# Kernel tuning notes

Measured on AMD Instinct MI355X. Metric: run time of the kernel, lower is better.

## Reference

```python
import jax, jax.numpy as jnp
import numpy as np

D_MODEL = 512
N_HEADS = 8
D_K = D_MODEL // N_HEADS


def setup_inputs() -> dict:
    key = jax.random.key(0)
    ks = jax.random.split(key, 12)
    B, L = 2, 512
    s = 1.0 / np.sqrt(D_MODEL)
    sk = 1.0 / np.sqrt(D_K)
    return {
        "query": jax.random.normal(ks[0], (B, L, D_MODEL), jnp.float32),
        "key": jax.random.normal(ks[1], (B, L, D_MODEL), jnp.float32),
        "value": jax.random.normal(ks[2], (B, L, D_MODEL), jnp.float32),
        "Wq": jax.random.normal(ks[3], (D_MODEL, D_MODEL), jnp.float32) * s,
        "bq": jnp.zeros((D_MODEL,), jnp.float32),
        "Wk": jax.random.normal(ks[4], (D_MODEL, D_MODEL), jnp.float32) * s,
        "bk": jnp.zeros((D_MODEL,), jnp.float32),
        "Wv": jax.random.normal(ks[5], (D_MODEL, D_MODEL), jnp.float32) * s,
        "bv": jnp.zeros((D_MODEL,), jnp.float32),
        "Wo": jax.random.normal(ks[6], (D_MODEL, D_MODEL), jnp.float32) * s,
        "bo": jnp.zeros((D_MODEL,), jnp.float32),
        "Aq": jax.random.normal(ks[7], (D_K, D_K), jnp.float32) * sk,  # inner W_q (no bias)
        "Ak": jax.random.normal(ks[8], (D_K, D_K), jnp.float32) * sk,  # inner W_k (no bias)
        "av": jax.random.normal(ks[9], (D_K,), jnp.float32) * sk,      # inner v (d_k -> 1)
    }


def _split_heads(x):
    B, L, _ = x.shape
    return x.reshape(B, L, N_HEADS, D_K).transpose(0, 2, 1, 3)  # [B,H,L,dk]


def reference(query, key, value, Wq, bq, Wk, bk, Wv, bv, Wo, bo, Aq, Ak, av):
    # outer projections (torch Linear: x @ W.T + b)
    Q = _split_heads(query @ Wq.T + bq)   # [B,H,Lq,dk]
    K = _split_heads(key @ Wk.T + bk)     # [B,H,Lk,dk]
    V = _split_heads(value @ Wv.T + bv)   # [B,H,Lk,dk]
    # inner additive attention: e_ij = v^T tanh(Aq q_i + Ak k_j)
    qp = Q @ Aq.T                          # [B,H,Lq,dk]
    kp = K @ Ak.T                          # [B,H,Lk,dk]
    energy = jnp.tanh(qp[:, :, :, None, :] + kp[:, :, None, :, :])  # [B,H,Lq,Lk,dk]
    scores = jnp.einsum('bhqkd,d->bhqk', energy, av)
    attn = jax.nn.softmax(scores, axis=-1)  # dropout disabled (eval)
    out = jnp.einsum('bhqk,bhkd->bhqd', attn, V)  # [B,H,Lq,dk]
    B, _, Lq, _ = out.shape
    out = out.transpose(0, 2, 1, 3).reshape(B, Lq, D_MODEL)
    return out @ Wo.T + bo
```

## Files before the change

kernel.cpp:

```cpp
#include <hip/hip_runtime.h>

#define LOG2E 1.4426950408889634f

typedef __bf16 bf16x8 __attribute__((ext_vector_type(8)));
typedef float f32x4 __attribute__((ext_vector_type(4)));

__device__ __forceinline__ unsigned short bfb(__bf16 b){
  union { __bf16 b; unsigned short u; } z; z.b = b; return z.u;
}
__device__ __forceinline__ void split8(const float* p, bf16x8& hi, bf16x8& lo){
  #pragma unroll
  for (int j = 0; j < 8; j++){
    float f = p[j];
    __bf16 h = (__bf16)f;
    hi[j] = h;
    lo[j] = (__bf16)(f - (float)h);
  }
}


__global__ __launch_bounds__(256) void prep_all(
    const float* __restrict__ Wq, const float* __restrict__ Aq,
    const float* __restrict__ Wk, const float* __restrict__ Ak,
    const float* __restrict__ bq, const float* __restrict__ bk,
    const float* __restrict__ av,
    const float* __restrict__ Wv, const float* __restrict__ Wo,
    unsigned short* __restrict__ W2qp, unsigned short* __restrict__ W2kp,
    unsigned short* __restrict__ Wvp,  unsigned short* __restrict__ Wop,
    float* __restrict__ b2q, float* __restrict__ b2k, float* __restrict__ av2g){
  if (blockIdx.x >= 1024){
    if (blockIdx.x == 1280){
      if (blockIdx.y == 0){
        #pragma unroll
        for (int rep = 0; rep < 2; rep++){
          int n = rep * 256 + threadIdx.x;
          int h = n >> 6, e = n & 63;
          float aq = 0.f, ak = 0.f;
          for (int c = 0; c < 64; c++){
            aq += Aq[e*64 + c] * bq[h*64 + c];
            ak += Ak[e*64 + c] * bk[h*64 + c];
          }
          b2q[n] = aq * (2.f * LOG2E);
          b2k[n] = ak * (2.f * LOG2E);
        }
      } else {
        if (threadIdx.x < 64) av2g[threadIdx.x] = -2.f * LOG2E * av[threadIdx.x];
      }
      return;
    }
    const float* src = blockIdx.y ? Wo : Wv;
    unsigned short* dst = blockIdx.y ? Wop : Wvp;
    int base = ((blockIdx.x - 1024) * 256 + threadIdx.x) * 4;
    int n = base >> 9, k0 = base & 511;
    float4 v = *(const float4*)(src + base);
    ushort4 h, l;
    float f; __bf16 hb;
    f = v.x; hb = (__bf16)f; h.x = bfb(hb); l.x = bfb((__bf16)(f - (float)hb));
    f = v.y; hb = (__bf16)f; h.y = bfb(hb); l.y = bfb((__bf16)(f - (float)hb));
    f = v.z; hb = (__bf16)f; h.z = bfb(hb); l.z = bfb((__bf16)(f - (float)hb));
    f = v.w; hb = (__bf16)f; h.w = bfb(hb); l.w = bfb((__bf16)(f - (float)hb));
    int nt = n >> 4, ln = n & 15;
    int ks = k0 >> 5, q = (k0 & 31) >> 3, j0 = k0 & 7;
    size_t off = (size_t)((nt*16 + ks) * 2) * 512 + (q*16 + ln) * 8 + j0;
    *(ushort4*)(dst + off)       = h;
    *(ushort4*)(dst + off + 512) = l;
    return;
  }
  const float* W  = blockIdx.y ? Wk : Wq;
  const float* Am = blockIdx.y ? Ak : Aq;
  unsigned short* dst = blockIdx.y ? W2kp : W2qp;
  int idx = blockIdx.x * 256 + threadIdx.x;
  int n = idx >> 9, k = idx & 511;
  int h = n >> 6, e = n & 63;
  float acc = 0.f;
  #pragma unroll 8
  for (int c = 0; c < 64; c++)
    acc += Am[e*64 + c] * W[(h*64 + c)*512 + k];
  float v = acc * (2.f * LOG2E);
  __bf16 hb = (__bf16)v;
  int nt = n >> 4, ln = n & 15;
  int ks = k >> 5, q = (k & 31) >> 3, j = k & 7;
  size_t off = (size_t)((nt*16 + ks) * 2) * 512 + (q*16 + ln) * 8 + j;
  dst[off]       = bfb(hb);
  dst[off + 512] = bfb((__bf16)(v - (float)hb));
}

struct GemmBatch {
  const float* Af;
  const unsigned short* Bp;
  const float* bias;
  float* Cf;
  int transposed;
  int expout;
};
struct GemmArgs { GemmBatch g[3]; };

__global__ __launch_bounds__(256) void gemm_nk(GemmArgs ga){
  GemmBatch gb = ga.g[blockIdx.z];
  __shared__ float As[64 * 68];
  const int tid = threadIdx.x, lane = tid & 63, w = tid >> 6;
  const int l15 = lane & 15, quad = lane >> 4;
  const int m0  = blockIdx.x * 64;
  const int nt0 = blockIdx.y * 4;
  f32x4 ac0 = {0.f,0.f,0.f,0.f}, ac1 = ac0, ac2 = ac0, ac3 = ac0;

  const int sr = tid >> 2;
  const int sc = (tid & 3) * 16;
  const float* srcA = gb.Af + (size_t)(m0 + sr) * 512 + sc;
  float* dstA = &As[sr * 68 + sc];

  for (int kc = 0; kc < 8; kc++){
    __syncthreads();
    #pragma unroll
    for (int i = 0; i < 4; i++)
      *(f32x4*)(dstA + i*4) = *(const f32x4*)(srcA + kc*64 + i*4);
    __syncthreads();
    #pragma unroll
    for (int s = 0; s < 2; s++){
      int ks = kc * 2 + s;
      bf16x8 ah, al;
      split8(&As[(w*16 + l15) * 68 + s*32 + quad*8], ah, al);
      #pragma unroll
      for (int t = 0; t < 4; t++){
        const unsigned short* bp = gb.Bp + (size_t)(((nt0 + t)*16 + ks) * 2) * 512 + lane*8;
        bf16x8 bh = *(const bf16x8*)bp;
        bf16x8 bl = *(const bf16x8*)(bp + 512);
        f32x4& ac = (t==0)?ac0:(t==1)?ac1:(t==2)?ac2:ac3;
        ac = __builtin_amdgcn_mfma_f32_16x16x32_bf16(ah, bh, ac, 0, 0, 0);
        ac = __builtin_amdgcn_mfma_f32_16x16x32_bf16(al, bh, ac, 0, 0, 0);
        ac = __builtin_amdgcn_mfma_f32_16x16x32_bf16(ah, bl, ac, 0, 0, 0);
      }
    }
  }

  const int mrow = m0 + w * 16 + quad * 4;
  #pragma unroll
  for (int t = 0; t < 4; t++){
    f32x4 v = (t==0)?ac0:(t==1)?ac1:(t==2)?ac2:ac3;
    int n = nt0 * 16 + t * 16 + l15;
    float bs = gb.bias[n];
    #pragma unroll
    for (int r = 0; r < 4; r++){
      float val = v[r] + bs;
      if (gb.expout) val = __builtin_amdgcn_exp2f(val);
      int m2 = mrow + r;
      if (gb.transposed){
        gb.Cf[(size_t)(((m2 >> 9) * 8 + (n >> 6)) * 64 + (n & 63)) * 512 + (m2 & 511)] = val;
      } else {
        gb.Cf[(size_t)m2 * 512 + n] = val;
      }
    }
  }
}

__global__ __launch_bounds__(512, 4) void attn_kernel(
    const float* __restrict__ eqT, const float* __restrict__ ekp,
    const float* __restrict__ Vv, const float* __restrict__ av2g,
    float* __restrict__ Oh){
  __shared__ float bufA[64 * 130];
  __shared__ float bufB[64 * 130];
  __shared__ unsigned short pcb[2 * 16 * 136];
  __shared__ float dn[16];
  float* cmb = bufA;

  const int tid = threadIdx.x, lane = tid & 63, w = tid >> 6;
  const int l15 = lane & 15, quad = lane >> 4;
  const int bh = blockIdx.y;
  const int i0 = blockIdx.x * 16;
  const size_t kbase = (size_t)(bh >> 3) * 512 * 512 + (size_t)(bh & 7) * 64;
  const int r0 = __builtin_amdgcn_readfirstlane(2 * w);
  const size_t qbase = (size_t)bh * 64 * 512 + i0 + r0;
  const int ntile = w & 3, khalf = w >> 2;

  float den0 = 0.f, den1 = 0.f;
  f32x4 Cacc = {0.f, 0.f, 0.f, 0.f};

  {
    #pragma unroll
    for (int m = 0; m < 8; m++){
      int i = w + 8 * m;
      float a = ekp[kbase + (size_t)(2*i    ) * 512 + lane];
      float b = ekp[kbase + (size_t)(2*i + 1) * 512 + lane];
      *(float2*)&bufA[lane * 130 + 2*i] = make_float2(a, b);
    }
  }
  __syncthreads();

  for (int c = 0; c < 4; c++){
    float va[8], vb[8];
    #pragma unroll
    for (int m = 0; m < 8; m++){
      int i = w + 8 * m;
      va[m] = Vv[kbase + (size_t)(c*128 + 2*i    ) * 512 + lane];
      vb[m] = Vv[kbase + (size_t)(c*128 + 2*i + 1) * 512 + lane];
    }
    float s00 = 0.f, s01 = 0.f, s10 = 0.f, s11 = 0.f;
    #pragma unroll 4
    for (int d = 0; d < 64; d++){
      float2 eq = *(const float2*)(eqT + qbase + (size_t)d * 512);
      float a2 = av2g[d];
      float2 ek = *(const float2*)&bufA[d * 130 + 2 * lane];
      s00 += a2 * __builtin_amdgcn_rcpf(__builtin_fmaf(eq.x, ek.x, 1.f));
      s01 += a2 * __builtin_amdgcn_rcpf(__builtin_fmaf(eq.x, ek.y, 1.f));
      s10 += a2 * __builtin_amdgcn_rcpf(__builtin_fmaf(eq.y, ek.x, 1.f));
      s11 += a2 * __builtin_amdgcn_rcpf(__builtin_fmaf(eq.y, ek.y, 1.f));
    }
    float e00 = __builtin_amdgcn_exp2f(s00);
    float e01 = __builtin_amdgcn_exp2f(s01);
    float e10 = __builtin_amdgcn_exp2f(s10);
    float e11 = __builtin_amdgcn_exp2f(s11);
    den0 += e00 + e01; den1 += e10 + e11;
    {
      __bf16 h00 = (__bf16)e00, h01 = (__bf16)e01, h10 = (__bf16)e10, h11 = (__bf16)e11;
      ushort2 hi0 = { bfb(h00), bfb(h01) };
      ushort2 hi1 = { bfb(h10), bfb(h11) };
      ushort2 lo0 = { bfb((__bf16)(e00 - (float)h00)), bfb((__bf16)(e01 - (float)h01)) };
      ushort2 lo1 = { bfb((__bf16)(e10 - (float)h10)), bfb((__bf16)(e11 - (float)h11)) };
      *(ushort2*)&pcb[(0*16 + r0    ) * 136 + 2*lane] = hi0;
      *(ushort2*)&pcb[(0*16 + r0 + 1) * 136 + 2*lane] = hi1;
      *(ushort2*)&pcb[(1*16 + r0    ) * 136 + 2*lane] = lo0;
      *(ushort2*)&pcb[(1*16 + r0 + 1) * 136 + 2*lane] = lo1;
    }
    #pragma unroll
    for (int m = 0; m < 8; m++){
      int i = w + 8 * m;
      *(float2*)&bufB[lane * 130 + 2*i] = make_float2(va[m], vb[m]);
    }
    __syncthreads();

    float ka[8], kb[8];
    if (c < 3){
      #pragma unroll
      for (int m = 0; m < 8; m++){
        int i = w + 8 * m;
        ka[m] = ekp[kbase + (size_t)((c+1)*128 + 2*i    ) * 512 + lane];
        kb[m] = ekp[kbase + (size_t)((c+1)*128 + 2*i + 1) * 512 + lane];
      }
    }
    #pragma unroll
    for (int kk2 = 0; kk2 < 2; kk2++){
      int k0 = (khalf * 2 + kk2) * 32 + quad * 8;
      bf16x8 ph = *(const bf16x8*)&pcb[(0*16 + l15) * 136 + k0];
      bf16x8 pl = *(const bf16x8*)&pcb[(1*16 + l15) * 136 + k0];
      const float* vp = &bufB[(ntile*16 + l15) * 130 + k0];
      bf16x8 vh, vl;
      #pragma unroll
      for (int j = 0; j < 8; j++){
        float f = vp[j];
        __bf16 h = (__bf16)f;
        vh[j] = h; vl[j] = (__bf16)(f - (float)h);
      }
      Cacc = __builtin_amdgcn_mfma_f32_16x16x32_bf16(ph, vh, Cacc, 0, 0, 0);
      Cacc = __builtin_amdgcn_mfma_f32_16x16x32_bf16(pl, vh, Cacc, 0, 0, 0);
      Cacc = __builtin_amdgcn_mfma_f32_16x16x32_bf16(ph, vl, Cacc, 0, 0, 0);
    }
    if (c < 3){
      #pragma unroll
      for (int m = 0; m < 8; m++){
        int i = w + 8 * m;
        *(float2*)&bufA[lane * 130 + 2*i] = make_float2(ka[m], kb[m]);
      }
    }
    __syncthreads();
  }

  #pragma unroll
  for (int off = 1; off < 64; off <<= 1){
    den0 += __shfl_xor(den0, off, 64);
    den1 += __shfl_xor(den1, off, 64);
  }
  if (lane == 0){ dn[r0] = den0; dn[r0 + 1] = den1; }
  __syncthreads();
  if (w >= 4){
    #pragma unroll
    for (int r = 0; r < 4; r++) cmb[(w - 4) * 256 + lane * 4 + r] = Cacc[r];
  }
  __syncthreads();
  if (w < 4){
    #pragma unroll
    for (int r = 0; r < 4; r++){
      float cv = Cacc[r] + cmb[w * 256 + lane * 4 + r];
      int row = quad * 4 + r;
      int d = ntile * 16 + l15;
      Oh[kbase + (size_t)(i0 + row) * 512 + d] = cv / dn[row];
    }
  }
}

extern "C" void kernel_launch(void* const* d_in, const int* in_sizes, int n_in,
                              void* d_out, int out_size, void* d_ws, size_t ws_size,
                              hipStream_t stream){
  const float* q_in = (const float*)d_in[0];
  const float* k_in = (const float*)d_in[1];
  const float* v_in = (const float*)d_in[2];
  const float* Wq_  = (const float*)d_in[3];
  const float* bq_  = (const float*)d_in[4];
  const float* Wk_  = (const float*)d_in[5];
  const float* bk_  = (const float*)d_in[6];
  const float* Wv_  = (const float*)d_in[7];
  const float* bv_  = (const float*)d_in[8];
  const float* Wo_  = (const float*)d_in[9];
  const float* bo_  = (const float*)d_in[10];
  const float* Aq_  = (const float*)d_in[11];
  const float* Ak_  = (const float*)d_in[12];
  const float* av_  = (const float*)d_in[13];

  char* ws = (char*)d_ws;
  unsigned short* W2qp = (unsigned short*)(ws + 0);
  unsigned short* W2kp = (unsigned short*)(ws + 1048576);
  float* Oh = (float*)(ws + 0);
  unsigned short* Wvp = (unsigned short*)(ws + 2097152);
  unsigned short* Wop = (unsigned short*)(ws + 3145728);
  float* b2q  = (float*)(ws + 4194304);
  float* b2k  = (float*)(ws + 4196352);
  float* av2g = (float*)(ws + 4198400);
  float* eqT  = (float*)(ws + 4198656);
  float* ekp  = (float*)(ws + 6295808);
  float* Vw   = (float*)(ws + 8392960);

  prep_all<<<dim3(1281, 2, 1), 256, 0, stream>>>(Wq_, Aq_, Wk_, Ak_, bq_, bk_, av_,
                                                 Wv_, Wo_,
                                                 W2qp, W2kp, Wvp, Wop,
                                                 b2q, b2k, av2g);

  GemmArgs ga;
  ga.g[0] = { q_in, W2qp, b2q, eqT, 1, 1 };
  ga.g[1] = { k_in, W2kp, b2k, ekp, 0, 1 };
  ga.g[2] = { v_in, Wvp,  bv_, Vw,  0, 0 };
  gemm_nk<<<dim3(16, 8, 3), 256, 0, stream>>>(ga);

  attn_kernel<<<dim3(32, 16, 1), 512, 0, stream>>>(eqT, ekp, Vw, av2g, Oh);

  GemmArgs go;
  go.g[0] = { Oh, Wop, bo_, (float*)d_out, 0, 0 };
  go.g[1] = go.g[0];
  go.g[2] = go.g[0];
  gemm_nk<<<dim3(16, 8, 1), 256, 0, stream>>>(go);
}
```

Measured before the change: 169.6 us.

## Prepack V as bf16 hi/lo MFMA fragments and drop LDS staging in attention

The V projection GEMM now writes its output already split into bf16 hi/lo pairs in the MFMA B-operand layout, and K is stored transposed like Q. The attention kernel reads K and the prepacked V straight from global memory instead of staging them through LDS, and uses 256-thread blocks covering 8 query rows with a double-buffered probability tile, which removes one barrier per chunk and the cross-wave reduction. The intent is to cut LDS traffic, barriers and the repeated fp32-to-bf16 splitting of V. In exchange, half of each MFMA tile is zero padding (only 8 of 16 rows are used), so MFMA work per useful output doubles, the grid doubles, and K/V reads rely on the cache.

```diff
diff --git a/kernel.cpp b/kernel.cpp
--- a/kernel.cpp
+++ b/kernel.cpp
@@ -90,8 +90,10 @@
   const unsigned short* Bp;
   const float* bias;
   float* Cf;
+  unsigned short* Cb;
   int transposed;
   int expout;
+  int vpack;
 };
 struct GemmArgs { GemmBatch g[3]; };
 
@@ -134,72 +136,77 @@
   }
 
   const int mrow = m0 + w * 16 + quad * 4;
-  #pragma unroll
-  for (int t = 0; t < 4; t++){
-    f32x4 v = (t==0)?ac0:(t==1)?ac1:(t==2)?ac2:ac3;
-    int n = nt0 * 16 + t * 16 + l15;
-    float bs = gb.bias[n];
-    #pragma unroll
-    for (int r = 0; r < 4; r++){
-      float val = v[r] + bs;
-      if (gb.expout) val = __builtin_amdgcn_exp2f(val);
-      int m2 = mrow + r;
-      if (gb.transposed){
-        gb.Cf[(size_t)(((m2 >> 9) * 8 + (n >> 6)) * 64 + (n & 63)) * 512 + (m2 & 511)] = val;
-      } else {
-        gb.Cf[(size_t)m2 * 512 + n] = val;
+  if (gb.vpack){
+    int b = mrow >> 9;
+    int j = mrow & 511;
+    int ks = j >> 5, q = (j & 31) >> 3, jj0 = mrow & 7;
+    #pragma unroll
+    for (int t = 0; t < 4; t++){
+      f32x4 v = (t==0)?ac0:(t==1)?ac1:(t==2)?ac2:ac3;
+      int n = nt0 * 16 + t * 16 + l15;
+      float bs = gb.bias[n];
+      int h = n >> 6, dk = n & 63;
+      size_t base = ((size_t)(((b*8 + h)*4 + (dk >> 4))*16 + ks)*2)*512
+                  + (q*16 + (dk & 15))*8 + jj0;
+      ushort4 hh, ll;
+      float val; __bf16 hb;
+      val = v[0] + bs; hb = (__bf16)val; hh.x = bfb(hb); ll.x = bfb((__bf16)(val - (float)hb));
+      val = v[1] + bs; hb = (__bf16)val; hh.y = bfb(hb); ll.y = bfb((__bf16)(val - (float)hb));
+      val = v[2] + bs; hb = (__bf16)val; hh.z = bfb(hb); ll.z = bfb((__bf16)(val - (float)hb));
+      val = v[3] + bs; hb = (__bf16)val; hh.w = bfb(hb); ll.w = bfb((__bf16)(val - (float)hb));
+      *(ushort4*)(gb.Cb + base)       = hh;
+      *(ushort4*)(gb.Cb + base + 512) = ll;
+    }
+  } else {
+    #pragma unroll
+    for (int t = 0; t < 4; t++){
+      f32x4 v = (t==0)?ac0:(t==1)?ac1:(t==2)?ac2:ac3;
+      int n = nt0 * 16 + t * 16 + l15;
+      float bs = gb.bias[n];
+      #pragma unroll
+      for (int r = 0; r < 4; r++){
+        float val = v[r] + bs;
+        if (gb.expout) val = __builtin_amdgcn_exp2f(val);
+        int m2 = mrow + r;
+        if (gb.transposed){
+          gb.Cf[(size_t)(((m2 >> 9) * 8 + (n >> 6)) * 64 + (n & 63)) * 512 + (m2 & 511)] = val;
+        } else {
+          gb.Cf[(size_t)m2 * 512 + n] = val;
+        }
       }
     }
   }
 }
 
-__global__ __launch_bounds__(512, 4) void attn_kernel(
-    const float* __restrict__ eqT, const float* __restrict__ ekp,
-    const float* __restrict__ Vv, const float* __restrict__ av2g,
+__global__ __launch_bounds__(256, 4) void attn_kernel(
+    const float* __restrict__ eqT, const float* __restrict__ ekT,
+    const unsigned short* __restrict__ Vpk, const float* __restrict__ av2g,
     float* __restrict__ Oh){
-  __shared__ float bufA[64 * 130];
-  __shared__ float bufB[64 * 130];
-  __shared__ unsigned short pcb[2 * 16 * 136];
-  __shared__ float dn[16];
-  float* cmb = bufA;
+  __shared__ unsigned short pcb[2][2 * 16 * 136];
+  __shared__ float dn[8];
 
   const int tid = threadIdx.x, lane = tid & 63, w = tid >> 6;
   const int l15 = lane & 15, quad = lane >> 4;
   const int bh = blockIdx.y;
-  const int i0 = blockIdx.x * 16;
-  const size_t kbase = (size_t)(bh >> 3) * 512 * 512 + (size_t)(bh & 7) * 64;
+  const int i0 = blockIdx.x * 8;
+  const size_t obase = (size_t)(bh >> 3) * 512 * 512 + (size_t)(bh & 7) * 64;
+  const size_t tbase = (size_t)bh * 64 * 512;
   const int r0 = __builtin_amdgcn_readfirstlane(2 * w);
-  const size_t qbase = (size_t)bh * 64 * 512 + i0 + r0;
-  const int ntile = w & 3, khalf = w >> 2;
+  const int nt = w;
+
+  for (int t = tid; t < 2 * 2 * 16 * 136; t += 256) ((unsigned short*)pcb)[t] = 0;
+  __syncthreads();
 
   float den0 = 0.f, den1 = 0.f;
   f32x4 Cacc = {0.f, 0.f, 0.f, 0.f};
 
-  {
-    #pragma unroll
-    for (int m = 0; m < 8; m++){
-      int i = w + 8 * m;
-      float a = ekp[kbase + (size_t)(2*i    ) * 512 + lane];
-      float b = ekp[kbase + (size_t)(2*i + 1) * 512 + lane];
-      *(float2*)&bufA[lane * 130 + 2*i] = make_float2(a, b);
-    }
-  }
-  __syncthreads();
-
   for (int c = 0; c < 4; c++){
-    float va[8], vb[8];
-    #pragma unroll
-    for (int m = 0; m < 8; m++){
-      int i = w + 8 * m;
-      va[m] = Vv[kbase + (size_t)(c*128 + 2*i    ) * 512 + lane];
-      vb[m] = Vv[kbase + (size_t)(c*128 + 2*i + 1) * 512 + lane];
-    }
     float s00 = 0.f, s01 = 0.f, s10 = 0.f, s11 = 0.f;
-    #pragma unroll 4
+    #pragma unroll 8
     for (int d = 0; d < 64; d++){
-      float2 eq = *(const float2*)(eqT + qbase + (size_t)d * 512);
+      float2 eq = *(const float2*)(eqT + tbase + (size_t)d * 512 + i0 + r0);
+      float2 ek = *(const float2*)(ekT + tbase + (size_t)d * 512 + c*128 + 2*lane);
       float a2 = av2g[d];
-      float2 ek = *(const float2*)&bufA[d * 130 + 2 * lane];
       s00 += a2 * __builtin_amdgcn_rcpf(__builtin_fmaf(eq.x, ek.x, 1.f));
       s01 += a2 * __builtin_amdgcn_rcpf(__builtin_fmaf(eq.x, ek.y, 1.f));
       s10 += a2 * __builtin_amdgcn_rcpf(__builtin_fmaf(eq.y, ek.x, 1.f));
@@ -211,57 +218,34 @@
     float e11 = __builtin_amdgcn_exp2f(s11);
     den0 += e00 + e01; den1 += e10 + e11;
     {
+      unsigned short* pc = pcb[c & 1];
       __bf16 h00 = (__bf16)e00, h01 = (__bf16)e01, h10 = (__bf16)e10, h11 = (__bf16)e11;
       ushort2 hi0 = { bfb(h00), bfb(h01) };
       ushort2 hi1 = { bfb(h10), bfb(h11) };
       ushort2 lo0 = { bfb((__bf16)(e00 - (float)h00)), bfb((__bf16)(e01 - (float)h01)) };
       ushort2 lo1 = { bfb((__bf16)(e10 - (float)h10)), bfb((__bf16)(e11 - (float)h11)) };
-      *(ushort2*)&pcb[(0*16 + r0    ) * 136 + 2*lane] = hi0;
-      *(ushort2*)&pcb[(0*16 + r0 + 1) * 136 + 2*lane] = hi1;
-      *(ushort2*)&pcb[(1*16 + r0    ) * 136 + 2*lane] = lo0;
-      *(ushort2*)&pcb[(1*16 + r0 + 1) * 136 + 2*lane] = lo1;
-    }
-    #pragma unroll
-    for (int m = 0; m < 8; m++){
-      int i = w + 8 * m;
-      *(float2*)&bufB[lane * 130 + 2*i] = make_float2(va[m], vb[m]);
+      *(ushort2*)&pc[(0*16 + r0    ) * 136 + 2*lane] = hi0;
+      *(ushort2*)&pc[(0*16 + r0 + 1) * 136 + 2*lane] = hi1;
+      *(ushort2*)&pc[(1*16 + r0    ) * 136 + 2*lane] = lo0;
+      *(ushort2*)&pc[(1*16 + r0 + 1) * 136 + 2*lane] = lo1;
     }
     __syncthreads();
-
-    float ka[8], kb[8];
-    if (c < 3){
+    {
+      const unsigned short* pc = pcb[c & 1];
       #pragma unroll
-      for (int m = 0; m < 8; m++){
-        int i = w + 8 * m;
-        ka[m] = ekp[kbase + (size_t)((c+1)*128 + 2*i    ) * 512 + lane];
-        kb[m] = ekp[kbase + (size_t)((c+1)*128 + 2*i + 1) * 512 + lane];
+      for (int kk2 = 0; kk2 < 4; kk2++){
+        int ks = c * 4 + kk2;
+        const unsigned short* vp = Vpk + ((size_t)((bh*4 + nt)*16 + ks) * 2) * 512 + lane*8;
+        bf16x8 vh = *(const bf16x8*)vp;
+        bf16x8 vl = *(const bf16x8*)(vp + 512);
+        int k0 = kk2 * 32 + quad * 8;
+        bf16x8 ph = *(const bf16x8*)&pc[(0*16 + l15) * 136 + k0];
+        bf16x8 pl = *(const bf16x8*)&pc[(1*16 + l15) * 136 + k0];
+        Cacc = __builtin_amdgcn_mfma_f32_16x16x32_bf16(ph, vh, Cacc, 0, 0, 0);
+        Cacc = __builtin_amdgcn_mfma_f32_16x16x32_bf16(pl, vh, Cacc, 0, 0, 0);
+        Cacc = __builtin_amdgcn_mfma_f32_16x16x32_bf16(ph, vl, Cacc, 0, 0, 0);
       }
     }
-    #pragma unroll
-    for (int kk2 = 0; kk2 < 2; kk2++){
-      int k0 = (khalf * 2 + kk2) * 32 + quad * 8;
-      bf16x8 ph = *(const bf16x8*)&pcb[(0*16 + l15) * 136 + k0];
-      bf16x8 pl = *(const bf16x8*)&pcb[(1*16 + l15) * 136 + k0];
-      const float* vp = &bufB[(ntile*16 + l15) * 130 + k0];
-      bf16x8 vh, vl;
-      #pragma unroll
-      for (int j = 0; j < 8; j++){
-        float f = vp[j];
-        __bf16 h = (__bf16)f;
-        vh[j] = h; vl[j] = (__bf16)(f - (float)h);
-      }
-      Cacc = __builtin_amdgcn_mfma_f32_16x16x32_bf16(ph, vh, Cacc, 0, 0, 0);
-      Cacc = __builtin_amdgcn_mfma_f32_16x16x32_bf16(pl, vh, Cacc, 0, 0, 0);
-      Cacc = __builtin_amdgcn_mfma_f32_16x16x32_bf16(ph, vl, Cacc, 0, 0, 0);
-    }
-    if (c < 3){
-      #pragma unroll
-      for (int m = 0; m < 8; m++){
-        int i = w + 8 * m;
-        *(float2*)&bufA[lane * 130 + 2*i] = make_float2(ka[m], kb[m]);
-      }
-    }
-    __syncthreads();
   }
 
   #pragma unroll
@@ -271,18 +255,11 @@
   }
   if (lane == 0){ dn[r0] = den0; dn[r0 + 1] = den1; }
   __syncthreads();
-  if (w >= 4){
-    #pragma unroll
-    for (int r = 0; r < 4; r++) cmb[(w - 4) * 256 + lane * 4 + r] = Cacc[r];
-  }
-  __syncthreads();
-  if (w < 4){
+  if (quad < 2){
     #pragma unroll
     for (int r = 0; r < 4; r++){
-      float cv = Cacc[r] + cmb[w * 256 + lane * 4 + r];
       int row = quad * 4 + r;
-      int d = ntile * 16 + l15;
-      Oh[kbase + (size_t)(i0 + row) * 512 + d] = cv / dn[row];
+      Oh[obase + (size_t)(i0 + row) * 512 + nt * 16 + l15] = Cacc[r] / dn[row];
     }
   }
 }
@@ -315,8 +292,8 @@
   float* b2k  = (float*)(ws + 4196352);
   float* av2g = (float*)(ws + 4198400);
   float* eqT  = (float*)(ws + 4198656);
-  float* ekp  = (float*)(ws + 6295808);
-  float* Vw   = (float*)(ws + 8392960);
+  float* ekT  = (float*)(ws + 6295808);
+  unsigned short* Vpk = (unsigned short*)(ws + 8392960);
 
   prep_all<<<dim3(1281, 2, 1), 256, 0, stream>>>(Wq_, Aq_, Wk_, Ak_, bq_, bk_, av_,
                                                  Wv_, Wo_,
@@ -324,15 +301,15 @@
                                                  b2q, b2k, av2g);
 
   GemmArgs ga;
-  ga.g[0] = { q_in, W2qp, b2q, eqT, 1, 1 };
-  ga.g[1] = { k_in, W2kp, b2k, ekp, 0, 1 };
-  ga.g[2] = { v_in, Wvp,  bv_, Vw,  0, 0 };
+  ga.g[0] = { q_in, W2qp, b2q, eqT,    nullptr, 1, 1, 0 };
+  ga.g[1] = { k_in, W2kp, b2k, ekT,    nullptr, 1, 1, 0 };
+  ga.g[2] = { v_in, Wvp,  bv_, nullptr, Vpk,    0, 0, 1 };
   gemm_nk<<<dim3(16, 8, 3), 256, 0, stream>>>(ga);
 
-  attn_kernel<<<dim3(32, 16, 1), 512, 0, stream>>>(eqT, ekp, Vw, av2g, Oh);
+  attn_kernel<<<dim3(64, 16, 1), 256, 0, stream>>>(eqT, ekT, Vpk, av2g, Oh);
 
   GemmArgs go;
-  go.g[0] = { Oh, Wop, bo_, (float*)d_out, 0, 0 };
+  go.g[0] = { Oh, Wop, bo_, (float*)d_out, nullptr, 0, 0, 0 };
   go.g[1] = go.g[0];
   go.g[2] = go.g[0];
   gemm_nk<<<dim3(16, 8, 1), 256, 0, stream>>>(go);
```

Measured after the change: 172.5 us. No clear change (+1.7%).

## Emit V projection as pre-split bf16 MFMA fragments and load directly in attention

Applied to the files above, without the earlier changes.

The V projection GEMM epilogue now writes V as hi/lo bf16 pairs in the MFMA B-operand fragment layout, not as fp32. The attention kernel loads these fragments straight from global memory, dropping the per-chunk V staging through shared memory and the repeated fp32-to-bf16 split. This removes a shared buffer and the LDS traffic and conversion work in the attention loop, which could also raise occupancy. The cost is uncoalesced-looking 8-byte scattered stores in the GEMM epilogue and global-memory fragment loads on the MFMA critical path.

```diff
diff --git a/kernel.cpp b/kernel.cpp
--- a/kernel.cpp
+++ b/kernel.cpp
@@ -90,8 +90,10 @@
   const unsigned short* Bp;
   const float* bias;
   float* Cf;
+  unsigned short* Cb;
   int transposed;
   int expout;
+  int vpack;
 };
 struct GemmArgs { GemmBatch g[3]; };
 
@@ -134,20 +136,43 @@
   }
 
   const int mrow = m0 + w * 16 + quad * 4;
-  #pragma unroll
-  for (int t = 0; t < 4; t++){
-    f32x4 v = (t==0)?ac0:(t==1)?ac1:(t==2)?ac2:ac3;
-    int n = nt0 * 16 + t * 16 + l15;
-    float bs = gb.bias[n];
-    #pragma unroll
-    for (int r = 0; r < 4; r++){
-      float val = v[r] + bs;
-      if (gb.expout) val = __builtin_amdgcn_exp2f(val);
-      int m2 = mrow + r;
-      if (gb.transposed){
-        gb.Cf[(size_t)(((m2 >> 9) * 8 + (n >> 6)) * 64 + (n & 63)) * 512 + (m2 & 511)] = val;
-      } else {
-        gb.Cf[(size_t)m2 * 512 + n] = val;
+  if (gb.vpack){
+    int b = mrow >> 9;
+    int j = mrow & 511;
+    int ks = j >> 5, q = (j & 31) >> 3, jj0 = mrow & 7;
+    #pragma unroll
+    for (int t = 0; t < 4; t++){
+      f32x4 v = (t==0)?ac0:(t==1)?ac1:(t==2)?ac2:ac3;
+      int n = nt0 * 16 + t * 16 + l15;
+      float bs = gb.bias[n];
+      int h = n >> 6, dk = n & 63;
+      size_t base = ((size_t)(((b*8 + h)*4 + (dk >> 4))*16 + ks)*2)*512
+                  + (q*16 + (dk & 15))*8 + jj0;
+      ushort4 hh, ll;
+      float val; __bf16 hb;
+      val = v[0] + bs; hb = (__bf16)val; hh.x = bfb(hb); ll.x = bfb((__bf16)(val - (float)hb));
+      val = v[1] + bs; hb = (__bf16)val; hh.y = bfb(hb); ll.y = bfb((__bf16)(val - (float)hb));
+      val = v[2] + bs; hb = (__bf16)val; hh.z = bfb(hb); ll.z = bfb((__bf16)(val - (float)hb));
+      val = v[3] + bs; hb = (__bf16)val; hh.w = bfb(hb); ll.w = bfb((__bf16)(val - (float)hb));
+      *(ushort4*)(gb.Cb + base)       = hh;
+      *(ushort4*)(gb.Cb + base + 512) = ll;
+    }
+  } else {
+    #pragma unroll
+    for (int t = 0; t < 4; t++){
+      f32x4 v = (t==0)?ac0:(t==1)?ac1:(t==2)?ac2:ac3;
+      int n = nt0 * 16 + t * 16 + l15;
+      float bs = gb.bias[n];
+      #pragma unroll
+      for (int r = 0; r < 4; r++){
+        float val = v[r] + bs;
+        if (gb.expout) val = __builtin_amdgcn_exp2f(val);
+        int m2 = mrow + r;
+        if (gb.transposed){
+          gb.Cf[(size_t)(((m2 >> 9) * 8 + (n >> 6)) * 64 + (n & 63)) * 512 + (m2 & 511)] = val;
+        } else {
+          gb.Cf[(size_t)m2 * 512 + n] = val;
+        }
       }
     }
   }
@@ -155,10 +180,9 @@
 
 __global__ __launch_bounds__(512, 4) void attn_kernel(
     const float* __restrict__ eqT, const float* __restrict__ ekp,
-    const float* __restrict__ Vv, const float* __restrict__ av2g,
+    const unsigned short* __restrict__ Vpk, const float* __restrict__ av2g,
     float* __restrict__ Oh){
   __shared__ float bufA[64 * 130];
-  __shared__ float bufB[64 * 130];
   __shared__ unsigned short pcb[2 * 16 * 136];
   __shared__ float dn[16];
   float* cmb = bufA;
@@ -187,13 +211,6 @@
   __syncthreads();
 
   for (int c = 0; c < 4; c++){
-    float va[8], vb[8];
-    #pragma unroll
-    for (int m = 0; m < 8; m++){
-      int i = w + 8 * m;
-      va[m] = Vv[kbase + (size_t)(c*128 + 2*i    ) * 512 + lane];
-      vb[m] = Vv[kbase + (size_t)(c*128 + 2*i + 1) * 512 + lane];
-    }
     float s00 = 0.f, s01 = 0.f, s10 = 0.f, s11 = 0.f;
     #pragma unroll 4
     for (int d = 0; d < 64; d++){
@@ -221,11 +238,6 @@
       *(ushort2*)&pcb[(1*16 + r0    ) * 136 + 2*lane] = lo0;
       *(ushort2*)&pcb[(1*16 + r0 + 1) * 136 + 2*lane] = lo1;
     }
-    #pragma unroll
-    for (int m = 0; m < 8; m++){
-      int i = w + 8 * m;
-      *(float2*)&bufB[lane * 130 + 2*i] = make_float2(va[m], vb[m]);
-    }
     __syncthreads();
 
     float ka[8], kb[8];
@@ -239,17 +251,13 @@
     }
     #pragma unroll
     for (int kk2 = 0; kk2 < 2; kk2++){
+      int ks = c * 4 + khalf * 2 + kk2;
+      const unsigned short* vp = Vpk + ((size_t)((bh*4 + ntile)*16 + ks) * 2) * 512 + lane*8;
+      bf16x8 vh = *(const bf16x8*)vp;
+      bf16x8 vl = *(const bf16x8*)(vp + 512);
       int k0 = (khalf * 2 + kk2) * 32 + quad * 8;
       bf16x8 ph = *(const bf16x8*)&pcb[(0*16 + l15) * 136 + k0];
       bf16x8 pl = *(const bf16x8*)&pcb[(1*16 + l15) * 136 + k0];
-      const float* vp = &bufB[(ntile*16 + l15) * 130 + k0];
-      bf16x8 vh, vl;
-      #pragma unroll
-      for (int j = 0; j < 8; j++){
-        float f = vp[j];
-        __bf16 h = (__bf16)f;
-        vh[j] = h; vl[j] = (__bf16)(f - (float)h);
-      }
       Cacc = __builtin_amdgcn_mfma_f32_16x16x32_bf16(ph, vh, Cacc, 0, 0, 0);
       Cacc = __builtin_amdgcn_mfma_f32_16x16x32_bf16(pl, vh, Cacc, 0, 0, 0);
       Cacc = __builtin_amdgcn_mfma_f32_16x16x32_bf16(ph, vl, Cacc, 0, 0, 0);
@@ -316,7 +324,7 @@
   float* av2g = (float*)(ws + 4198400);
   float* eqT  = (float*)(ws + 4198656);
   float* ekp  = (float*)(ws + 6295808);
-  float* Vw   = (float*)(ws + 8392960);
+  unsigned short* Vpk = (unsigned short*)(ws + 8392960);
 
   prep_all<<<dim3(1281, 2, 1), 256, 0, stream>>>(Wq_, Aq_, Wk_, Ak_, bq_, bk_, av_,
                                                  Wv_, Wo_,
@@ -324,15 +332,15 @@
                                                  b2q, b2k, av2g);
 
   GemmArgs ga;
-  ga.g[0] = { q_in, W2qp, b2q, eqT, 1, 1 };
-  ga.g[1] = { k_in, W2kp, b2k, ekp, 0, 1 };
-  ga.g[2] = { v_in, Wvp,  bv_, Vw,  0, 0 };
+  ga.g[0] = { q_in, W2qp, b2q, eqT,    nullptr, 1, 1, 0 };
+  ga.g[1] = { k_in, W2kp, b2k, ekp,    nullptr, 0, 1, 0 };
+  ga.g[2] = { v_in, Wvp,  bv_, nullptr, Vpk,    0, 0, 1 };
   gemm_nk<<<dim3(16, 8, 3), 256, 0, stream>>>(ga);
 
-  attn_kernel<<<dim3(32, 16, 1), 512, 0, stream>>>(eqT, ekp, Vw, av2g, Oh);
+  attn_kernel<<<dim3(32, 16, 1), 512, 0, stream>>>(eqT, ekp, Vpk, av2g, Oh);
 
   GemmArgs go;
-  go.g[0] = { Oh, Wop, bo_, (float*)d_out, 0, 0 };
+  go.g[0] = { Oh, Wop, bo_, (float*)d_out, nullptr, 0, 0, 0 };
   go.g[1] = go.g[0];
   go.g[2] = go.g[0];
   gemm_nk<<<dim3(16, 8, 1), 256, 0, stream>>>(go);
```

Result: no change. 170.1 us (+0.3%).
